# Kernel tuning notes

Hardware: AMD Instinct MI355X
Metric: run time of the kernel (lower is better)

Reference implementation:

```python
import jax, jax.numpy as jnp
import numpy as np

NUM_USER = 20000
NUM_ITEM = 40000
N_NODES = NUM_USER + NUM_ITEM
DIM = 64
V_DIM = 2048
T_DIM = 768
N_EDGES = 1_000_000
K_USER = 40
K_ITEM = 10
N_LAYERS = 2


def setup_inputs() -> dict:
    key = jax.random.key(0)
    ks = iter(jax.random.split(key, 32))

    def xavier(shape):
        s = (2.0 / (shape[0] + shape[-1])) ** 0.5
        return jax.random.normal(next(ks), shape, jnp.float32) * s

    # bipartite user-item interactions, doubled (undirected), as in DRAGON.__init__
    u = jax.random.randint(next(ks), (N_EDGES,), 0, NUM_USER)
    it = jax.random.randint(next(ks), (N_EDGES,), NUM_USER, N_NODES)
    edge_index = jnp.stack([jnp.concatenate([u, it]), jnp.concatenate([it, u])])

    v_feat = jax.random.normal(next(ks), (NUM_ITEM, V_DIM), jnp.float32)
    t_feat = jax.random.normal(next(ks), (NUM_ITEM, T_DIM), jnp.float32)

    # KNN item-item adjacency (top-10 per row) with symmetric-normalized values,
    # mirroring get_knn_adj_mat/compute_normalized_laplacian
    rows = jnp.repeat(jnp.arange(NUM_ITEM), K_ITEM)
    cols = jax.random.randint(next(ks), (NUM_ITEM * K_ITEM,), 0, NUM_ITEM)
    mm_indices = jnp.stack([rows, cols])
    row_sum = jax.ops.segment_sum(jnp.ones(NUM_ITEM * K_ITEM, jnp.float32), rows,
                                  num_segments=NUM_ITEM) + 1e-7
    rinv = row_sum ** -0.5
    mm_values = rinv[rows] * rinv[cols]

    user_graph = jax.random.randint(next(ks), (NUM_USER, K_USER), 0, NUM_USER)
    user_weight_matrix = jax.nn.softmax(
        jax.random.normal(next(ks), (NUM_USER, K_USER), jnp.float32), axis=1)
    weight_u = jax.nn.softmax(
        jax.random.normal(next(ks), (NUM_USER, 2, 1), jnp.float32), axis=1)

    return {
        'edge_index': edge_index,
        'v_feat': v_feat, 't_feat': t_feat,
        'v_pref': xavier((NUM_USER, DIM)), 't_pref': xavier((NUM_USER, DIM)),
        'v_mlp1_w': xavier((V_DIM, 4 * DIM)), 'v_mlp1_b': jnp.zeros(4 * DIM, jnp.float32),
        'v_mlp2_w': xavier((4 * DIM, DIM)), 'v_mlp2_b': jnp.zeros(DIM, jnp.float32),
        't_mlp1_w': xavier((T_DIM, 4 * DIM)), 't_mlp1_b': jnp.zeros(4 * DIM, jnp.float32),
        't_mlp2_w': xavier((4 * DIM, DIM)), 't_mlp2_b': jnp.zeros(DIM, jnp.float32),
        'v_conv_w': xavier((DIM, DIM)), 'v_conv_b': jnp.zeros(DIM, jnp.float32),
        't_conv_w': xavier((DIM, DIM)), 't_conv_b': jnp.zeros(DIM, jnp.float32),
        'weight_u': weight_u,
        'user_graph': user_graph,
        'user_weight_matrix': user_weight_matrix,
        'mm_indices': mm_indices,
        'mm_values': mm_values,
    }


def _l2n(x):
    n = jnp.linalg.norm(x, axis=-1, keepdims=True)
    return x / jnp.maximum(n, 1e-12)


def reference(edge_index, v_feat, t_feat, v_pref, t_pref,
              v_mlp1_w, v_mlp1_b, v_mlp2_w, v_mlp2_b,
              t_mlp1_w, t_mlp1_b, t_mlp2_w, t_mlp2_b,
              v_conv_w, v_conv_b, t_conv_w, t_conv_b,
              weight_u, user_graph, user_weight_matrix,
              mm_indices, mm_values):
    seg = jax.ops.segment_sum
    # GCNConv normalization with self-loops (shared by both branches)
    sl = jnp.arange(N_NODES)
    src = jnp.concatenate([edge_index[0], sl])
    dst = jnp.concatenate([edge_index[1], sl])
    deg = seg(jnp.ones_like(dst, dtype=jnp.float32), dst, num_segments=N_NODES)
    dinv = deg ** -0.5
    norm = (dinv[src] * dinv[dst])[:, None]

    def conv(x, w, b):  # out[dst] += norm * (x @ w)[src], then bias
        return seg(norm * (x @ w)[src], dst, num_segments=N_NODES) + b

    def branch(feat, pref, w1, b1, w2, b2, cw, cb):
        temp = jax.nn.leaky_relu(feat @ w1 + b1) @ w2 + b2  # [I, D]
        x = _l2n(jnp.concatenate([pref, temp], axis=0))      # [N, D]
        h = conv(x, cw, cb)
        h1 = conv(h, cw, cb)
        return x + h + h1

    v_rep = branch(v_feat, v_pref, v_mlp1_w, v_mlp1_b, v_mlp2_w, v_mlp2_b, v_conv_w, v_conv_b)
    t_rep = branch(t_feat, t_pref, t_mlp1_w, t_mlp1_b, t_mlp2_w, t_mlp2_b, t_conv_w, t_conv_b)

    representation = jnp.concatenate([v_rep, t_rep], axis=1)  # [N, 2D]
    wu = weight_u[:, :, 0]  # [U, 2]
    user_rep = jnp.concatenate([wu[:, 0:1] * v_rep[:NUM_USER],
                                wu[:, 1:2] * t_rep[:NUM_USER]], axis=1)  # [U, 2D]
    item_rep = representation[NUM_USER:]  # [I, 2D]

    # User_Graph_sample: weighted sum over sampled user neighborhoods
    h_u = jnp.einsum('uk,ukd->ud', user_weight_matrix, user_rep[user_graph])
    user_rep = user_rep + h_u

    # n_layers of sparse Laplacian propagation over KNN item-item graph
    row, col = mm_indices[0], mm_indices[1]
    h_i = item_rep
    for _ in range(N_LAYERS):
        h_i = seg(mm_values[:, None] * h_i[col], row, num_segments=NUM_ITEM)
    item_rep = item_rep + h_i

    return jnp.concatenate([user_rep, item_rep], axis=0)  # [N, 2D]
```

## Files before the change

### kernel.cpp

```cpp
#include <hip/hip_runtime.h>

#define NUSER 20000
#define NITEM 40000
#define NNODE 60000
#define DIM   64
#define NE    1000000
#define KUSER 40
#define KITEM 10

typedef __attribute__((ext_vector_type(8))) short short8v;
typedef __attribute__((ext_vector_type(4))) float floatx4;

__device__ inline short bf16rne(float f) {
    unsigned u = __builtin_bit_cast(unsigned, f);
    unsigned r = (u + 0x7fffu + ((u >> 16) & 1u)) >> 16;
    return (short)r;
}
__device__ inline unsigned cvt_pk_bf16(float lo, float hi) {
    unsigned r;
    asm("v_cvt_pk_bf16_f32 %0, %1, %2" : "=v"(r) : "v"(lo), "v"(hi));
    return r;
}
__device__ inline float bflo(unsigned v) { return __builtin_bit_cast(float, v << 16); }
__device__ inline float bfhi(unsigned v) { return __builtin_bit_cast(float, v & 0xffff0000u); }

__global__ __launch_bounds__(256) void k_count_pair(const int* __restrict__ uu, const int* __restrict__ it,
                                                    int* __restrict__ cnt) {
    int i = blockIdx.x * 256 + threadIdx.x;
    if (i >= NE) return;
    atomicAdd(&cnt[uu[i]], 1);
    atomicAdd(&cnt[it[i]], 1);
}

__global__ __launch_bounds__(256) void k_scanA(const int* __restrict__ v, int* __restrict__ excl,
                                               int* __restrict__ bsum, float* __restrict__ dinv, int n) {
    __shared__ int s[256];
    int t = threadIdx.x, i = blockIdx.x * 256 + t;
    int orig = (i < n) ? v[i] : 0;
    if (i < n) dinv[i] = 1.0f / sqrtf((float)(orig + 1));
    s[t] = orig; __syncthreads();
    #pragma unroll
    for (int off = 1; off < 256; off <<= 1) {
        int u = (t >= off) ? s[t - off] : 0;
        __syncthreads();
        s[t] += u;
        __syncthreads();
    }
    if (i < n) excl[i] = s[t] - orig;
    if (t == 255) bsum[blockIdx.x] = s[255];
}

__global__ __launch_bounds__(256) void k_scanB(int* __restrict__ bsum, int nb) {
    __shared__ int s[256];
    int t = threadIdx.x;
    int orig = (t < nb) ? bsum[t] : 0;
    s[t] = orig; __syncthreads();
    #pragma unroll
    for (int off = 1; off < 256; off <<= 1) {
        int u = (t >= off) ? s[t - off] : 0;
        __syncthreads();
        s[t] += u;
        __syncthreads();
    }
    if (t < nb) bsum[t] = s[t] - orig;
}

__global__ __launch_bounds__(256) void k_scanC(int* __restrict__ excl, const int* __restrict__ bsum,
                                               int* __restrict__ cursor, int n) {
    int i = blockIdx.x * 256 + threadIdx.x;
    if (i < n) {
        int v = excl[i] + bsum[blockIdx.x];
        excl[i] = v;
        cursor[i] = v;
    }
    if (i == 0) excl[n] = 2 * NE;
}

__global__ __launch_bounds__(256) void k_fill_pair(const int* __restrict__ uu, const int* __restrict__ it,
                                                   const float* __restrict__ dinv, int* __restrict__ cursor,
                                                   unsigned* __restrict__ csr_pkd) {
    int i = blockIdx.x * 256 + threadIdx.x;
    if (i >= NE) return;
    int u = uu[i], t = it[i];
    unsigned pku = ((unsigned)(unsigned short)bf16rne(dinv[u]) << 16) | (unsigned)u;
    unsigned pkt = ((unsigned)(unsigned short)bf16rne(dinv[t]) << 16) | (unsigned)t;
    int pos1 = atomicAdd(&cursor[t], 1);
    csr_pkd[pos1] = pku;
    int pos2 = atomicAdd(&cursor[u], 1);
    csr_pkd[pos2] = pkt;
}

__global__ __launch_bounds__(256) void k_transpose_all(const float* __restrict__ W1v, const float* __restrict__ W1t,
                                                       const float* __restrict__ W2v, const float* __restrict__ W2t,
                                                       short* __restrict__ Bv, short* __restrict__ Bt,
                                                       short* __restrict__ B2v, short* __restrict__ B2t) {
    __shared__ float s[16][17];
    int bid = blockIdx.x;
    const float* B; short* D; int K, N, local;
    if (bid < 2048)      { B = W1v; D = Bv;  K = 2048; N = 256; local = bid; }
    else if (bid < 2816) { B = W1t; D = Bt;  K = 768;  N = 256; local = bid - 2048; }
    else if (bid < 2880) { B = W2v; D = B2v; K = 256;  N = 64;  local = bid - 2816; }
    else                 { B = W2t; D = B2t; K = 256;  N = 64;  local = bid - 2880; }
    int ktiles = K >> 4;
    int k0 = (local % ktiles) * 16, n0 = (local / ktiles) * 16;
    int t = threadIdx.x, tx = t & 15, ty = t >> 4;
    s[ty][tx] = B[(size_t)(k0 + ty) * N + n0 + tx];
    __syncthreads();
    int k = k0 + tx, n = n0 + ty;
    D[(size_t)(k >> 5) * (N * 32) + n * 32 + (k & 31)] = bf16rne(s[tx][ty]);
}

__global__ __launch_bounds__(256) void k_prep(const float* __restrict__ Wv, const float* __restrict__ Wt,
                                              const float* __restrict__ bv, const float* __restrict__ bt,
                                              short* __restrict__ Bcat, float* __restrict__ bw, float* __restrict__ bb) {
    __shared__ float Wld[2][64][65];
    __shared__ float W2ld[2][64][65];
    int t = threadIdx.x;
    for (int id = t; id < 8192; id += 256) {
        int z = id >> 12, k = (id >> 6) & 63, n = id & 63;
        Wld[z][k][n] = (z ? Wt : Wv)[k * 64 + n];
    }
    __syncthreads();
    for (int id = t; id < 8192; id += 256) {
        int z = id >> 12, k = (id >> 6) & 63, n = id & 63;
        float a = 0.f;
        #pragma unroll 8
        for (int m = 0; m < 64; m++) a += Wld[z][k][m] * Wld[z][m][n];
        W2ld[z][k][n] = a;
    }
    __syncthreads();
    for (int id = t; id < 32768; id += 256) {
        int k = id >> 7, n = id & 127;
        int kb = k >> 6, kk = k & 63;
        float v = 0.f;
        if (kb == 0)      { if (n < 64)  v = Wld[0][kk][n]; }
        else if (kb == 1) { if (n >= 64) v = Wld[1][kk][n - 64]; }
        else if (kb == 2) { if (n < 64)  v = W2ld[0][kk][n]; }
        else              { if (n >= 64) v = W2ld[1][kk][n - 64]; }
        Bcat[(k >> 5) * 4096 + n * 32 + (k & 31)] = bf16rne(v);
    }
    if (t < 128) {
        int z = t >> 6, n = t & 63;
        const float* b = z ? bt : bv;
        float a = 0.f;
        #pragma unroll 8
        for (int k = 0; k < 64; k++) a += b[k] * Wld[z][k][n];
        bw[t] = a;
        bb[t] = 2.f * b[n];
    }
}

#define AP   40
#define MIDP 264
#define VBLKS (NITEM / 64)
__global__ __launch_bounds__(256) void mlp_merged(const float* __restrict__ Av, const float* __restrict__ At,
                                                  const short* __restrict__ B1v, const short* __restrict__ B1t,
                                                  const float* __restrict__ b1v, const float* __restrict__ b1t,
                                                  const short* __restrict__ B2v, const short* __restrict__ B2t,
                                                  const float* __restrict__ b2v, const float* __restrict__ b2t,
                                                  unsigned* __restrict__ xbf) {
    __shared__ short smem[2 * 64 * AP + 2 * 256 * AP];
    short* As = smem;
    short* Bs = smem + 2 * 64 * AP;
    const bool isV = blockIdx.x < VBLKS;
    const float* A    = isV ? Av : At;
    const short* B1t_ = isV ? B1v : B1t;
    const float* b1   = isV ? b1v : b1t;
    const short* B2t_ = isV ? B2v : B2t;
    const float* b2   = isV ? b2v : b2t;
    const int K = isV ? 2048 : 768;
    const int boff = isV ? 0 : 32;
    const int rowBase = (isV ? blockIdx.x : blockIdx.x - VBLKS) * 64;

    const int tid = threadIdx.x;
    const int lane = tid & 63, wid = tid >> 6;
    const int sar = tid >> 2, sac = (tid & 3) * 8;
    const float* aptr = A + (size_t)(rowBase + sar) * K + sac;

    const int fk = (lane >> 4) * 8;
    const int faoff = (lane & 15) * AP + fk;
    const int fboff = (wid * 64 + (lane & 15)) * AP + fk;

    floatx4 acc[4][4];
    #pragma unroll
    for (int m = 0; m < 4; m++)
        #pragma unroll
        for (int n = 0; n < 4; n++) acc[m][n] = (floatx4)0.f;

    float4 ra0, ra1;
    short8v rb[4];
    const int nk = K >> 5;

    auto ldg = [&](int ks) {
        const float* ap = aptr + ks * 32;
        ra0 = *(const float4*)(ap);
        ra1 = *(const float4*)(ap + 4);
        const short* bsrc = B1t_ + (size_t)ks * 8192 + tid * 8;
        #pragma unroll
        for (int it = 0; it < 4; it++) rb[it] = *(const short8v*)(bsrc + it * 2048);
    };
    auto stv = [&](int buf) {
        uint4 av;
        av.x = cvt_pk_bf16(ra0.x, ra0.y); av.y = cvt_pk_bf16(ra0.z, ra0.w);
        av.z = cvt_pk_bf16(ra1.x, ra1.y); av.w = cvt_pk_bf16(ra1.z, ra1.w);
        *(uint4*)&As[buf * (64 * AP) + sar * AP + sac] = av;
        #pragma unroll
        for (int it = 0; it < 4; it++)
            *(short8v*)&Bs[buf * (256 * AP) + (sar + it * 64) * AP + sac] = rb[it];
    };

    ldg(0); stv(0);
    __syncthreads();
    int cur = 0;
    for (int ks = 0; ks < nk; ++ks) {
        if (ks + 1 < nk) ldg(ks + 1);
        short8v a[4], b[4];
        #pragma unroll
        for (int m = 0; m < 4; m++) a[m] = *(const short8v*)&As[cur * (64 * AP) + faoff + m * 16 * AP];
        #pragma unroll
        for (int n = 0; n < 4; n++) b[n] = *(const short8v*)&Bs[cur * (256 * AP) + fboff + n * 16 * AP];
        #pragma unroll
        for (int m = 0; m < 4; m++)
            #pragma unroll
            for (int n = 0; n < 4; n++)
                acc[m][n] = __builtin_amdgcn_mfma_f32_16x16x32_bf16(a[m], b[n], acc[m][n], 0, 0, 0);
        if (ks + 1 < nk) stv(cur ^ 1);
        __syncthreads();
        cur ^= 1;
    }

    short* mid = Bs;
    float bcol[4];
    #pragma unroll
    for (int n = 0; n < 4; n++) bcol[n] = b1[wid * 64 + n * 16 + (lane & 15)];
    #pragma unroll
    for (int m = 0; m < 4; m++)
        #pragma unroll
        for (int n = 0; n < 4; n++)
            #pragma unroll
            for (int q = 0; q < 4; q++) {
                int row = m * 16 + (lane >> 4) * 4 + q;
                int col = wid * 64 + n * 16 + (lane & 15);
                float v = acc[m][n][q] + bcol[n];
                v = v > 0.f ? v : 0.01f * v;
                mid[row * MIDP + col] = bf16rne(v);
            }
    __syncthreads();

    floatx4 acc2[4];
    #pragma unroll
    for (int n2 = 0; n2 < 4; n2++) acc2[n2] = (floatx4)0.f;
    const int arow = wid * 16 + (lane & 15);
    #pragma unroll
    for (int ks2 = 0; ks2 < 8; ++ks2) {
        short8v af = *(const short8v*)&mid[arow * MIDP + ks2 * 32 + fk];
        const short* bp = B2t_ + ks2 * 2048 + fk;
        short8v bf4[4];
        #pragma unroll
        for (int n2 = 0; n2 < 4; n2++) bf4[n2] = *(const short8v*)(bp + (n2 * 16 + (lane & 15)) * 32);
        #pragma unroll
        for (int n2 = 0; n2 < 4; n2++)
            acc2[n2] = __builtin_amdgcn_mfma_f32_16x16x32_bf16(af, bf4[n2], acc2[n2], 0, 0, 0);
    }

    float b2c[4];
    #pragma unroll
    for (int n2 = 0; n2 < 4; n2++) b2c[n2] = b2[n2 * 16 + (lane & 15)];
    #pragma unroll
    for (int q = 0; q < 4; ++q) {
        float v[4]; float ss = 0.f;
        #pragma unroll
        for (int n2 = 0; n2 < 4; n2++) { v[n2] = acc2[n2][q] + b2c[n2]; ss += v[n2] * v[n2]; }
        ss += __shfl_xor(ss, 1, 64);
        ss += __shfl_xor(ss, 2, 64);
        ss += __shfl_xor(ss, 4, 64);
        ss += __shfl_xor(ss, 8, 64);
        float sc = 1.f / fmaxf(sqrtf(ss), 1e-12f);
        int grow = NUSER + rowBase + wid * 16 + (lane >> 4) * 4 + q;
        #pragma unroll
        for (int n2 = 0; n2 < 4; n2++) {
            float xn = v[n2] * sc;
            float pn = __shfl_xor(xn, 1, 64);
            if (!(lane & 1))
                xbf[(size_t)grow * 64 + boff + n2 * 8 + ((lane & 15) >> 1)] = cvt_pk_bf16(xn, pn);
        }
    }
}

__global__ __launch_bounds__(256) void k_l2n_pref(const float* __restrict__ prefv, const float* __restrict__ preft,
                                                  unsigned* __restrict__ xbf) {
    int row = blockIdx.x * 4 + (threadIdx.x >> 6);
    int lane = threadIdx.x & 63;
    if (row >= NUSER) return;
    const float* p = blockIdx.y ? preft : prefv;
    float v = p[(size_t)row * 64 + lane];
    float ss = v * v;
    #pragma unroll
    for (int off = 32; off >= 1; off >>= 1) ss += __shfl_xor(ss, off, 64);
    float xn = v / fmaxf(sqrtf(ss), 1e-12f);
    float pn = __shfl_xor(xn, 1, 64);
    if (!(lane & 1))
        xbf[(size_t)row * 64 + (blockIdx.y ? 32 : 0) + (lane >> 1)] = cvt_pk_bf16(xn, pn);
}

__global__ __launch_bounds__(256) void k_gather_p(const int* __restrict__ rowptr, const unsigned* __restrict__ csr_pkd,
                                                  const float* __restrict__ dinv, const unsigned* __restrict__ in_bf,
                                                  unsigned* __restrict__ out_bf, float* __restrict__ s_out) {
    int row = blockIdx.x * 4 + (threadIdx.x >> 6);
    int lane = threadIdx.x & 63;
    if (row >= NNODE) return;
    int p0 = rowptr[row], p1 = rowptr[row + 1];
    float dr = dinv[row];
    unsigned sv = in_bf[(size_t)row * 64 + lane];
    float ax0 = dr * bflo(sv), ay0 = dr * bfhi(sv);
    float ax1 = 0.f, ay1 = 0.f;
    float wsum = 0.f;
    for (int p = p0; p < p1; p += 64) {
        int c = p1 - p; if (c > 64) c = 64;
        unsigned pk = (lane < c) ? csr_pkd[p + lane] : 0u;
        wsum += bfhi(pk);
        int j = 0;
        for (; j + 4 <= c; j += 4) {
            unsigned e0 = __shfl(pk, j, 64),     e1 = __shfl(pk, j + 1, 64);
            unsigned e2 = __shfl(pk, j + 2, 64), e3 = __shfl(pk, j + 3, 64);
            unsigned v0 = in_bf[(size_t)(e0 & 0xffffu) * 64 + lane];
            unsigned v1 = in_bf[(size_t)(e1 & 0xffffu) * 64 + lane];
            unsigned v2 = in_bf[(size_t)(e2 & 0xffffu) * 64 + lane];
            unsigned v3 = in_bf[(size_t)(e3 & 0xffffu) * 64 + lane];
            float w0 = bfhi(e0), w1 = bfhi(e1), w2 = bfhi(e2), w3 = bfhi(e3);
            ax0 += w0 * bflo(v0); ay0 += w0 * bfhi(v0);
            ax1 += w1 * bflo(v1); ay1 += w1 * bfhi(v1);
            ax0 += w2 * bflo(v2); ay0 += w2 * bfhi(v2);
            ax1 += w3 * bflo(v3); ay1 += w3 * bfhi(v3);
        }
        for (; j < c; ++j) {
            unsigned e = __shfl(pk, j, 64);
            unsigned v = in_bf[(size_t)(e & 0xffffu) * 64 + lane];
            float w = bfhi(e);
            ax0 += w * bflo(v); ay0 += w * bfhi(v);
        }
    }
    out_bf[(size_t)row * 64 + lane] = cvt_pk_bf16(dr * (ax0 + ax1), dr * (ay0 + ay1));
    #pragma unroll
    for (int o = 32; o >= 1; o >>= 1) wsum += __shfl_xor(wsum, o, 64);
    if (lane == 0) s_out[row] = dr * (dr + wsum);
}

__global__ __launch_bounds__(512) void k_gather2_rep(const int* __restrict__ rowptr, const unsigned* __restrict__ csr_pkd,
                                                     const float* __restrict__ dinv, const unsigned* __restrict__ g1,
                                                     const short* __restrict__ Bcat, const unsigned* __restrict__ x_bf,
                                                     const float* __restrict__ s, const float* __restrict__ bw,
                                                     const float* __restrict__ bb, const float* __restrict__ weight_u,
                                                     float* __restrict__ rep0, unsigned* __restrict__ rep_bf) {
    __shared__ short As[16 * 264];
    const int tid = threadIdx.x, lane = tid & 63, w = tid >> 6;
    const int rowBase = blockIdx.x * 16;

    for (int rr = 0; rr < 2; ++rr) {
        int lrow = w * 2 + rr;
        int row = rowBase + lrow;
        int p0 = rowptr[row], p1 = rowptr[row + 1];
        float dr = dinv[row];
        unsigned sv = g1[(size_t)row * 64 + lane];
        float ax0 = dr * bflo(sv), ay0 = dr * bfhi(sv);
        float ax1 = 0.f, ay1 = 0.f;
        for (int p = p0; p < p1; p += 64) {
            int c = p1 - p; if (c > 64) c = 64;
            unsigned pk = (lane < c) ? csr_pkd[p + lane] : 0u;
            int j = 0;
            for (; j + 4 <= c; j += 4) {
                unsigned e0 = __shfl(pk, j, 64),     e1 = __shfl(pk, j + 1, 64);
                unsigned e2 = __shfl(pk, j + 2, 64), e3 = __shfl(pk, j + 3, 64);
                unsigned v0 = g1[(size_t)(e0 & 0xffffu) * 64 + lane];
                unsigned v1 = g1[(size_t)(e1 & 0xffffu) * 64 + lane];
                unsigned v2 = g1[(size_t)(e2 & 0xffffu) * 64 + lane];
                unsigned v3 = g1[(size_t)(e3 & 0xffffu) * 64 + lane];
                float w0 = bfhi(e0), w1 = bfhi(e1), w2 = bfhi(e2), w3 = bfhi(e3);
                ax0 += w0 * bflo(v0); ay0 += w0 * bfhi(v0);
                ax1 += w1 * bflo(v1); ay1 += w1 * bfhi(v1);
                ax0 += w2 * bflo(v2); ay0 += w2 * bfhi(v2);
                ax1 += w3 * bflo(v3); ay1 += w3 * bfhi(v3);
            }
            for (; j < c; ++j) {
                unsigned e = __shfl(pk, j, 64);
                unsigned v = g1[(size_t)(e & 0xffffu) * 64 + lane];
                float wj = bfhi(e);
                ax0 += wj * bflo(v); ay0 += wj * bfhi(v);
            }
        }
        *(unsigned*)&As[lrow * 264 + 2 * lane] = sv;
        *(unsigned*)&As[lrow * 264 + 128 + 2 * lane] = cvt_pk_bf16(dr * (ax0 + ax1), dr * (ay0 + ay1));
    }
    __syncthreads();

    const int fk = (lane >> 4) * 8;
    floatx4 acc = (floatx4)0.f;
    #pragma unroll
    for (int ks = 0; ks < 8; ++ks) {
        short8v af = *(const short8v*)&As[(lane & 15) * 264 + ks * 32 + fk];
        short8v bf = *(const short8v*)(Bcat + ks * 4096 + (w * 16 + (lane & 15)) * 32 + fk);
        acc = __builtin_amdgcn_mfma_f32_16x16x32_bf16(af, bf, acc, 0, 0, 0);
    }
    const int col = w * 16 + (lane & 15);
    const float bwc = bw[col], bbc = bb[col];
    #pragma unroll
    for (int q = 0; q < 4; ++q) {
        int lrow = (lane >> 4) * 4 + q;
        int row = rowBase + lrow;
        unsigned xw = x_bf[(size_t)row * 64 + (col >> 1)];
        float xval = (col & 1) ? bfhi(xw) : bflo(xw);
        float v = acc[q] + xval + s[row] * bwc + bbc;
        float wu = (row < NUSER) ? weight_u[row * 2 + (col >> 6)] : 1.0f;
        v *= wu;
        rep0[(size_t)row * 128 + col] = v;
        float pn = __shfl_xor(v, 1, 64);
        if (!(lane & 1))
            rep_bf[(size_t)row * 64 + (col >> 1)] = cvt_pk_bf16(v, pn);
    }
}

#define UBLK (NUSER * 64 / 256)
__global__ __launch_bounds__(256) void k_user_item1(const float* __restrict__ rep0, const unsigned* __restrict__ rep_bf,
                                                    const int* __restrict__ ug, const float* __restrict__ uwm,
                                                    const int* __restrict__ mm_col, const float* __restrict__ mm_values,
                                                    float* __restrict__ out, unsigned* __restrict__ tmp_bf) {
    int bid = blockIdx.x;
    if (bid < UBLK) {
        int id = bid * 256 + threadIdx.x;
        int u = id >> 6, lane = id & 63;
        float2 acc = *(const float2*)(rep0 + (size_t)u * 128 + 2 * lane);
        #pragma unroll 4
        for (int k = 0; k < KUSER; k++) {
            int nb = ug[u * KUSER + k];
            float w = uwm[u * KUSER + k];
            unsigned v = rep_bf[(size_t)nb * 64 + lane];
            acc.x += w * bflo(v);
            acc.y += w * bfhi(v);
        }
        *(float2*)(out + (size_t)u * 128 + 2 * lane) = acc;
    } else {
        int id = (bid - UBLK) * 256 + threadIdx.x;
        int r = id >> 6, lane = id & 63;
        float ax = 0.f, ay = 0.f;
        #pragma unroll
        for (int j = 0; j < KITEM; j++) {
            int c = mm_col[r * KITEM + j];
            float w = mm_values[r * KITEM + j];
            unsigned v = rep_bf[(size_t)(NUSER + c) * 64 + lane];
            ax += w * bflo(v);
            ay += w * bfhi(v);
        }
        tmp_bf[(size_t)r * 64 + lane] = cvt_pk_bf16(ax, ay);
    }
}

__global__ __launch_bounds__(256) void k_item2(const float* __restrict__ rep0, const unsigned* __restrict__ tmp_bf,
                                               const int* __restrict__ mm_col, const float* __restrict__ mm_values,
                                               float* __restrict__ out) {
    int id = blockIdx.x * 256 + threadIdx.x;
    int r = id >> 6, lane = id & 63;
    if (r >= NITEM) return;
    float ax = 0.f, ay = 0.f;
    #pragma unroll
    for (int j = 0; j < KITEM; j++) {
        int c = mm_col[r * KITEM + j];
        float w = mm_values[r * KITEM + j];
        unsigned v = tmp_bf[(size_t)c * 64 + lane];
        ax += w * bflo(v);
        ay += w * bfhi(v);
    }
    float2 base = *(const float2*)(rep0 + (size_t)(NUSER + r) * 128 + 2 * lane);
    float2 o;
    o.x = base.x + ax;
    o.y = base.y + ay;
    *(float2*)(out + (size_t)(NUSER + r) * 128 + 2 * lane) = o;
}

extern "C" void kernel_launch(void* const* d_in, const int* in_sizes, int n_in,
                              void* d_out, int out_size, void* d_ws, size_t ws_size,
                              hipStream_t stream) {
    const int*   edge_index = (const int*)d_in[0];
    const float* v_feat   = (const float*)d_in[1];
    const float* t_feat   = (const float*)d_in[2];
    const float* v_pref   = (const float*)d_in[3];
    const float* t_pref   = (const float*)d_in[4];
    const float* v_mlp1_w = (const float*)d_in[5];
    const float* v_mlp1_b = (const float*)d_in[6];
    const float* v_mlp2_w = (const float*)d_in[7];
    const float* v_mlp2_b = (const float*)d_in[8];
    const float* t_mlp1_w = (const float*)d_in[9];
    const float* t_mlp1_b = (const float*)d_in[10];
    const float* t_mlp2_w = (const float*)d_in[11];
    const float* t_mlp2_b = (const float*)d_in[12];
    const float* v_conv_w = (const float*)d_in[13];
    const float* v_conv_b = (const float*)d_in[14];
    const float* t_conv_w = (const float*)d_in[15];
    const float* t_conv_b = (const float*)d_in[16];
    const float* weight_u = (const float*)d_in[17];
    const int*   user_graph = (const int*)d_in[18];
    const float* uwm      = (const float*)d_in[19];
    const int*   mm_indices = (const int*)d_in[20];
    const float* mm_values  = (const float*)d_in[21];
    float* out = (float*)d_out;

    char* wsb = (char*)d_ws;
    size_t off = 0;
    auto alloc = [&](size_t bytes) -> void* {
        void* p = wsb + off;
        off = (off + bytes + 255) & ~(size_t)255;
        return p;
    };
    int*      cnt     = (int*)     alloc(NNODE * 4);
    float*    dinv    = (float*)   alloc(NNODE * 4);
    int*      rowptr  = (int*)     alloc((NNODE + 1) * 4);
    int*      bsum    = (int*)     alloc(256 * 4);
    int*      cursor  = (int*)     alloc(NNODE * 4);
    unsigned* csr_pkd = (unsigned*)alloc((size_t)2 * NE * 4);
    short*    Btw_v   = (short*)   alloc((size_t)2048 * 256 * 2);
    short*    Btw_t   = (short*)   alloc((size_t)768 * 256 * 2);
    short*    W2b_v   = (short*)   alloc((size_t)256 * 64 * 2);
    short*    W2b_t   = (short*)   alloc((size_t)256 * 64 * 2);
    short*    Bcat    = (short*)   alloc((size_t)256 * 128 * 2);
    float*    bw      = (float*)   alloc(128 * 4);
    float*    bb      = (float*)   alloc(128 * 4);
    float*    svec    = (float*)   alloc(NNODE * 4);
    unsigned* x_bf    = (unsigned*)alloc((size_t)NNODE * 64 * 4);
    unsigned* g1      = (unsigned*)alloc((size_t)NNODE * 64 * 4);
    float*    rep0    = (float*)   alloc((size_t)NNODE * 128 * 4);
    unsigned* rep_bf  = (unsigned*)alloc((size_t)NNODE * 64 * 4);
    unsigned* tmp_bf  = (unsigned*)alloc((size_t)NITEM * 64 * 4);
    (void)ws_size; (void)n_in; (void)in_sizes; (void)out_size;

    const int* pairs_u  = edge_index;
    const int* pairs_it = edge_index + NE;
    const int* mm_col = mm_indices + NITEM * KITEM;

    const int NB = (NNODE + 255) / 256;

    hipMemsetAsync(cnt, 0, NNODE * 4, stream);
    k_count_pair<<<(NE + 255) / 256, 256, 0, stream>>>(pairs_u, pairs_it, cnt);
    k_scanA<<<NB, 256, 0, stream>>>(cnt, rowptr, bsum, dinv, NNODE);
    k_scanB<<<1, 256, 0, stream>>>(bsum, NB);
    k_scanC<<<NB, 256, 0, stream>>>(rowptr, bsum, cursor, NNODE);
    k_fill_pair<<<(NE + 255) / 256, 256, 0, stream>>>(pairs_u, pairs_it, dinv, cursor, csr_pkd);

    k_prep<<<1, 256, 0, stream>>>(v_conv_w, t_conv_w, v_conv_b, t_conv_b, Bcat, bw, bb);
    k_transpose_all<<<2944, 256, 0, stream>>>(v_mlp1_w, t_mlp1_w, v_mlp2_w, t_mlp2_w,
                                              Btw_v, Btw_t, W2b_v, W2b_t);

    mlp_merged<<<2 * VBLKS, 256, 0, stream>>>(v_feat, t_feat, Btw_v, Btw_t, v_mlp1_b, t_mlp1_b,
                                              W2b_v, W2b_t, v_mlp2_b, t_mlp2_b, x_bf);
    {
        dim3 g(NUSER / 4, 2);
        k_l2n_pref<<<g, 256, 0, stream>>>(v_pref, t_pref, x_bf);
    }

    k_gather_p<<<(NNODE + 3) / 4, 256, 0, stream>>>(rowptr, csr_pkd, dinv, x_bf, g1, svec);
    k_gather2_rep<<<NNODE / 16, 512, 0, stream>>>(rowptr, csr_pkd, dinv, g1, Bcat, x_bf,
                                                  svec, bw, bb, weight_u, rep0, rep_bf);

    k_user_item1<<<UBLK + NITEM * 64 / 256, 256, 0, stream>>>(rep0, rep_bf, user_graph, uwm,
                                                              mm_col, mm_values, out, tmp_bf);
    k_item2<<<NITEM * 64 / 256, 256, 0, stream>>>(rep0, tmp_bf, mm_col, mm_values, out);
}
```

Measured before the change: 582.4 us.

## Enlarge MLP GEMM tile to 128 rows with 512-thread blocks

The fused two-layer MLP kernel now processes 128 feature rows per block using 8 waves arranged 2x4, instead of 64 rows with 4 waves. Each B weight tile loaded into shared memory is reused across twice as many rows, which halves weight traffic per row and halves the block count. The intermediate buffer is written as packed bf16 pairs through lane shuffles, and rows beyond the item count are clamped on load and masked on store. In exchange, shared memory per block grows and fewer blocks fit per CU, which may lower occupancy and latency hiding.

```diff
diff --git a/kernel.cpp b/kernel.cpp
--- a/kernel.cpp
+++ b/kernel.cpp
@@ -152,16 +152,17 @@
 
 #define AP   40
 #define MIDP 264
-#define VBLKS (NITEM / 64)
-__global__ __launch_bounds__(256) void mlp_merged(const float* __restrict__ Av, const float* __restrict__ At,
+#define MBLK 128
+#define VBLKS ((NITEM + MBLK - 1) / MBLK)
+__global__ __launch_bounds__(512, 4) void mlp_merged(const float* __restrict__ Av, const float* __restrict__ At,
                                                   const short* __restrict__ B1v, const short* __restrict__ B1t,
                                                   const float* __restrict__ b1v, const float* __restrict__ b1t,
                                                   const short* __restrict__ B2v, const short* __restrict__ B2t,
                                                   const float* __restrict__ b2v, const float* __restrict__ b2t,
                                                   unsigned* __restrict__ xbf) {
-    __shared__ short smem[2 * 64 * AP + 2 * 256 * AP];
+    __shared__ short smem[MBLK * MIDP];
     short* As = smem;
-    short* Bs = smem + 2 * 64 * AP;
+    short* Bs = smem + 2 * MBLK * AP;
     const bool isV = blockIdx.x < VBLKS;
     const float* A    = isV ? Av : At;
     const short* B1t_ = isV ? B1v : B1t;
@@ -170,16 +171,19 @@
     const float* b2   = isV ? b2v : b2t;
     const int K = isV ? 2048 : 768;
     const int boff = isV ? 0 : 32;
-    const int rowBase = (isV ? blockIdx.x : blockIdx.x - VBLKS) * 64;
+    const int rowBase = (isV ? blockIdx.x : blockIdx.x - VBLKS) * MBLK;
 
     const int tid = threadIdx.x;
     const int lane = tid & 63, wid = tid >> 6;
+    const int wr = wid >> 2, wc = wid & 3;
+
     const int sar = tid >> 2, sac = (tid & 3) * 8;
-    const float* aptr = A + (size_t)(rowBase + sar) * K + sac;
+    int aclamp = rowBase + sar; if (aclamp > NITEM - 1) aclamp = NITEM - 1;
+    const float* aptr = A + (size_t)aclamp * K + sac;
 
     const int fk = (lane >> 4) * 8;
-    const int faoff = (lane & 15) * AP + fk;
-    const int fboff = (wid * 64 + (lane & 15)) * AP + fk;
+    const int faoff = (wr * 64 + (lane & 15)) * AP + fk;
+    const int fboff = (wc * 64 + (lane & 15)) * AP + fk;
 
     floatx4 acc[4][4];
     #pragma unroll
@@ -188,25 +192,25 @@
         for (int n = 0; n < 4; n++) acc[m][n] = (floatx4)0.f;
 
     float4 ra0, ra1;
-    short8v rb[4];
+    short8v rb0, rb1;
     const int nk = K >> 5;
 
     auto ldg = [&](int ks) {
         const float* ap = aptr + ks * 32;
         ra0 = *(const float4*)(ap);
         ra1 = *(const float4*)(ap + 4);
-        const short* bsrc = B1t_ + (size_t)ks * 8192 + tid * 8;
-        #pragma unroll
-        for (int it = 0; it < 4; it++) rb[it] = *(const short8v*)(bsrc + it * 2048);
+        const short* bsrc = B1t_ + (size_t)ks * 8192 + tid * 16;
+        rb0 = *(const short8v*)(bsrc);
+        rb1 = *(const short8v*)(bsrc + 8);
     };
     auto stv = [&](int buf) {
         uint4 av;
         av.x = cvt_pk_bf16(ra0.x, ra0.y); av.y = cvt_pk_bf16(ra0.z, ra0.w);
         av.z = cvt_pk_bf16(ra1.x, ra1.y); av.w = cvt_pk_bf16(ra1.z, ra1.w);
-        *(uint4*)&As[buf * (64 * AP) + sar * AP + sac] = av;
-        #pragma unroll
-        for (int it = 0; it < 4; it++)
-            *(short8v*)&Bs[buf * (256 * AP) + (sar + it * 64) * AP + sac] = rb[it];
+        *(uint4*)&As[buf * (MBLK * AP) + sar * AP + sac] = av;
+        short* bd = &Bs[buf * (256 * AP) + (tid >> 1) * AP + (tid & 1) * 16];
+        *(short8v*)(bd) = rb0;
+        *(short8v*)(bd + 8) = rb1;
     };
 
     ldg(0); stv(0);
@@ -216,7 +220,7 @@
         if (ks + 1 < nk) ldg(ks + 1);
         short8v a[4], b[4];
         #pragma unroll
-        for (int m = 0; m < 4; m++) a[m] = *(const short8v*)&As[cur * (64 * AP) + faoff + m * 16 * AP];
+        for (int m = 0; m < 4; m++) a[m] = *(const short8v*)&As[cur * (MBLK * AP) + faoff + m * 16 * AP];
         #pragma unroll
         for (int n = 0; n < 4; n++) b[n] = *(const short8v*)&Bs[cur * (256 * AP) + fboff + n * 16 * AP];
         #pragma unroll
@@ -229,24 +233,27 @@
         cur ^= 1;
     }
 
-    short* mid = Bs;
+    unsigned* mid32 = (unsigned*)smem;
     float bcol[4];
     #pragma unroll
-    for (int n = 0; n < 4; n++) bcol[n] = b1[wid * 64 + n * 16 + (lane & 15)];
+    for (int n = 0; n < 4; n++) bcol[n] = b1[wc * 64 + n * 16 + (lane & 15)];
     #pragma unroll
     for (int m = 0; m < 4; m++)
         #pragma unroll
-        for (int n = 0; n < 4; n++)
+        for (int n = 0; n < 4; n++) {
+            int col = wc * 64 + n * 16 + (lane & 15);
             #pragma unroll
             for (int q = 0; q < 4; q++) {
-                int row = m * 16 + (lane >> 4) * 4 + q;
-                int col = wid * 64 + n * 16 + (lane & 15);
+                int row = wr * 64 + m * 16 + (lane >> 4) * 4 + q;
                 float v = acc[m][n][q] + bcol[n];
                 v = v > 0.f ? v : 0.01f * v;
-                mid[row * MIDP + col] = bf16rne(v);
+                float pn = __shfl_xor(v, 1, 64);
+                if (!(lane & 1)) mid32[row * 132 + (col >> 1)] = cvt_pk_bf16(v, pn);
             }
+        }
     __syncthreads();
 
+    const short* mid = smem;
     floatx4 acc2[4];
     #pragma unroll
     for (int n2 = 0; n2 < 4; n2++) acc2[n2] = (floatx4)0.f;
@@ -276,12 +283,14 @@
         ss += __shfl_xor(ss, 4, 64);
         ss += __shfl_xor(ss, 8, 64);
         float sc = 1.f / fmaxf(sqrtf(ss), 1e-12f);
-        int grow = NUSER + rowBase + wid * 16 + (lane >> 4) * 4 + q;
+        int lr = wid * 16 + (lane >> 4) * 4 + q;
+        int grow = NUSER + rowBase + lr;
+        bool ok = (rowBase + lr) < NITEM;
         #pragma unroll
         for (int n2 = 0; n2 < 4; n2++) {
             float xn = v[n2] * sc;
             float pn = __shfl_xor(xn, 1, 64);
-            if (!(lane & 1))
+            if (ok && !(lane & 1))
                 xbf[(size_t)grow * 64 + boff + n2 * 8 + ((lane & 15) >> 1)] = cvt_pk_bf16(xn, pn);
         }
     }
@@ -548,7 +557,7 @@
     k_transpose_all<<<2944, 256, 0, stream>>>(v_mlp1_w, t_mlp1_w, v_mlp2_w, t_mlp2_w,
                                               Btw_v, Btw_t, W2b_v, W2b_t);
 
-    mlp_merged<<<2 * VBLKS, 256, 0, stream>>>(v_feat, t_feat, Btw_v, Btw_t, v_mlp1_b, t_mlp1_b,
+    mlp_merged<<<2 * VBLKS, 512, 0, stream>>>(v_feat, t_feat, Btw_v, Btw_t, v_mlp1_b, t_mlp1_b,
                                               W2b_v, W2b_t, v_mlp2_b, t_mlp2_b, x_bf);
     {
         dim3 g(NUSER / 4, 2);
```

New measurement: 567.0 us. 1.03x faster.
